# Kernel optimization log

Hardware: AMD Instinct MI355X
Metric: run time of the kernel (lower is better)

Reference implementation:

```python
import jax, jax.numpy as jnp
import numpy as np

B, T, V, D, H, HS, FF, L = 4, 1024, 32000, 1024, 16, 64, 4096, 8
STD = 0.02

def _ln(x, g, b, eps=1e-5):
    m = x.mean(-1, keepdims=True)
    v = ((x - m) ** 2).mean(-1, keepdims=True)
    return (x - m) / jnp.sqrt(v + eps) * g + b

def setup_inputs() -> dict:
    key = jax.random.key(0)
    ks = jax.random.split(key, 16)
    n = lambda k, shp: jax.random.normal(k, shp, dtype=jnp.float32) * STD
    inp = {
        "idx": jax.random.randint(ks[0], (B, T), 0, V),
        "tok_emb": n(ks[1], (V, D)),
        "pos_emb": n(ks[2], (T, D)),
        # per-layer stacked attention weights; [D, H, HS] per layer (no bias)
        "Wq": n(ks[3], (L, D, H, HS)),
        "Wk": n(ks[4], (L, D, H, HS)),
        "Wv": n(ks[5], (L, D, H, HS)),
        "Wp": n(ks[6], (L, H * HS, D)),
        "bp": jnp.zeros((L, D), jnp.float32),
        "ln1_g": jnp.ones((L, D), jnp.float32),
        "ln1_b": jnp.zeros((L, D), jnp.float32),
        "ln2_g": jnp.ones((L, D), jnp.float32),
        "ln2_b": jnp.zeros((L, D), jnp.float32),
        "W1": n(ks[7], (L, D, FF)),
        "b1": jnp.zeros((L, FF), jnp.float32),
        "W2": n(ks[8], (L, FF, D)),
        "b2": jnp.zeros((L, D), jnp.float32),
        "lnf_g": jnp.ones((D,), jnp.float32),
        "lnf_b": jnp.zeros((D,), jnp.float32),
        "Wlm": n(ks[9], (D, V)),
        "blm": jnp.zeros((V,), jnp.float32),
    }
    return inp

def reference(idx, tok_emb, pos_emb, Wq, Wk, Wv, Wp, bp, ln1_g, ln1_b,
              ln2_g, ln2_b, W1, b1, W2, b2, lnf_g, lnf_b, Wlm, blm):
    Bb, Tt = idx.shape
    x = tok_emb[idx] + pos_emb[:Tt]                      # [B,T,D]
    causal = jnp.tril(jnp.ones((Tt, Tt), bool))          # tril mask
    for l in range(L):
        xn = _ln(x, ln1_g[l], ln1_b[l])
        q = jnp.einsum('btd,dhk->bhtk', xn, Wq[l])
        k = jnp.einsum('btd,dhk->bhtk', xn, Wk[l])
        v = jnp.einsum('btd,dhk->bhtk', xn, Wv[l])
        w = jnp.einsum('bhtk,bhsk->bhts', q, k) * (HS ** -0.5)
        w = jnp.where(causal, w, -jnp.inf)
        w = jax.nn.softmax(w, axis=-1)
        o = jnp.einsum('bhts,bhsk->bhtk', w, v)
        o = o.transpose(0, 2, 1, 3).reshape(Bb, Tt, H * HS)  # concat heads
        x = x + o @ Wp[l] + bp[l]
        xn = _ln(x, ln2_g[l], ln2_b[l])
        x = x + jax.nn.relu(xn @ W1[l] + b1[l]) @ W2[l] + b2[l]
    x = _ln(x, lnf_g, lnf_b)
    logits = x @ Wlm + blm                               # [B,T,V]
    return logits
```

## Files before the change

kernel.cpp:

```cpp
#include <hip/hip_runtime.h>
#include <cstdint>

typedef __attribute__((ext_vector_type(4))) float f32x4;
typedef __attribute__((ext_vector_type(8))) short s16x8;
typedef __attribute__((ext_vector_type(4))) short s16x4;
typedef unsigned short u16;
typedef unsigned int u32;
typedef __attribute__((address_space(1))) void gas_void;
typedef __attribute__((address_space(3))) void las_void;

#define B_ 4
#define T_ 1024
#define V_ 32000
#define D_ 1024
#define H_ 16
#define HS_ 64
#define FF_ 4096
#define L_ 8
#define BT_ (B_ * T_)

__device__ __forceinline__ float bf2f(u16 h) { return __uint_as_float(((u32)h) << 16); }
__device__ __forceinline__ u16 f2bf(float f) {
  u32 u = __float_as_uint(f);
  u += 0x7fffu + ((u >> 16) & 1u);
  return (u16)(u >> 16);
}

__device__ __forceinline__ void gld16(const void* g, void* l) {
  __builtin_amdgcn_global_load_lds((gas_void*)(uintptr_t)g,
                                   (las_void*)(u32)(uintptr_t)l, 16, 0, 0);
}


template <int EPI>
__global__ __launch_bounds__(512, 2) void gemm256(
    const u16* __restrict__ A, const u16* __restrict__ Bt,
    const float* __restrict__ bias, float* Cf, u16* Cb,
    int M, int N, int K, int nrowb) {
  __shared__ u16 lds[2][2][2][8192];
  const int tid = threadIdx.x;
  const int lane = tid & 63;
  const int lr = lane & 15, hi = lane >> 4;
  const int wid = tid >> 6;
  const int wm128 = (wid >> 2) << 7;
  const int wn64 = (wid & 3) << 6;
  const int logical = ((int)blockIdx.x & 7) * ((int)gridDim.x >> 3) + ((int)blockIdx.x >> 3);
  const int row0 = (logical % nrowb) << 8;
  const int col0 = (logical / nrowb) << 8;
  const int NT = K >> 6;
  const int srow = tid >> 2;
  const int schunk = tid & 3;
  const int xo = ((hi + (lr >> 1)) & 3) << 4;

  f32x4 acc[32];
#pragma unroll
  for (int i = 0; i < 32; ++i) acc[i] = f32x4{0.f, 0.f, 0.f, 0.f};
  s16x8 bfr[4];

#define VMW(N) asm volatile("s_waitcnt vmcnt(" #N ")" ::: "memory")

#define STG(DB, DK, OP, KT)                                                    \
  {                                                                            \
    const u16* sp_ = (OP) ? Bt : A;                                            \
    const int base_ = (OP) ? col0 : row0;                                      \
    const int c0_ = ((KT) << 6) + ((DK) << 5);                                 \
    _Pragma("unroll")                                                          \
    for (int sh_ = 0; sh_ < 2; ++sh_) {                                        \
      const int rr_ = (sh_ << 7) + srow;                                       \
      const int ko_ = ((schunk - (rr_ >> 1)) & 3) << 3;                        \
      gld16(sp_ + (size_t)(base_ + rr_) * K + c0_ + ko_,                       \
            (char*)&lds[DB][DK][OP][0] + (sh_ << 13) + (wid << 10));           \
    }                                                                          \
  }

#define PHASE(BUF, MH, KS, LOADB, STG_STMT, VM_STMT)                           \
  {                                                                            \
    __builtin_amdgcn_sched_barrier(0);                                         \
    const char* As_ = (const char*)&lds[BUF][KS][0][0];                        \
    const char* Bs_ = (const char*)&lds[BUF][KS][1][0];                        \
    const int ra_ = wm128 + ((MH) << 6) + lr;                                  \
    s16x8 af_[4];                                                              \
    _Pragma("unroll")                                                          \
    for (int q_ = 0; q_ < 4; ++q_)                                             \
      af_[q_] = *(const s16x8*)(As_ + ((ra_ + (q_ << 4)) << 6) + xo);          \
    if (LOADB) {                                                               \
      _Pragma("unroll")                                                        \
      for (int q_ = 0; q_ < 4; ++q_)                                           \
        bfr[q_] = *(const s16x8*)(Bs_ + ((wn64 + lr + (q_ << 4)) << 6) + xo);  \
    }                                                                          \
    STG_STMT;                                                                  \
    __builtin_amdgcn_sched_barrier(0);                                         \
    __builtin_amdgcn_s_barrier();                                              \
    asm volatile("s_waitcnt lgkmcnt(0)" ::: "memory");                         \
    __builtin_amdgcn_sched_barrier(0);                                         \
    __builtin_amdgcn_s_setprio(1);                                             \
    _Pragma("unroll")                                                          \
    for (int mi_ = 0; mi_ < 4; ++mi_) {                                        \
      _Pragma("unroll")                                                        \
      for (int nj_ = 0; nj_ < 4; ++nj_)                                        \
        acc[((MH)*4 + mi_) * 4 + nj_] = __builtin_amdgcn_mfma_f32_16x16x32_bf16( \
            af_[mi_], bfr[nj_], acc[((MH)*4 + mi_) * 4 + nj_], 0, 0, 0);       \
    }                                                                          \
    __builtin_amdgcn_s_setprio(0);                                             \
    __builtin_amdgcn_sched_barrier(0);                                         \
    VM_STMT;                                                                   \
    __builtin_amdgcn_s_barrier();                                              \
  }

  STG(0, 0, 0, 0)
  STG(0, 0, 1, 0)
  STG(0, 1, 0, 0)
  STG(0, 1, 1, 0)
  STG(1, 0, 0, 1)
  STG(1, 0, 1, 1)
  VMW(8);
  __builtin_amdgcn_s_barrier();

  const int NI = NT >> 1;
  for (int it = 0; it < NI - 1; ++it) {
    const int t1 = 2 * it + 1, t2 = 2 * it + 2, t3 = 2 * it + 3;
    PHASE(0, 0, 0, 1, STG(1, 1, 0, t1), )
    PHASE(0, 1, 0, 0, STG(1, 1, 1, t1), VMW(6))
    PHASE(0, 0, 1, 1, STG(0, 0, 0, t2), )
    PHASE(0, 1, 1, 0, STG(0, 0, 1, t2), VMW(6))
    PHASE(1, 0, 0, 1, STG(0, 1, 0, t2), )
    PHASE(1, 1, 0, 0, STG(0, 1, 1, t2), VMW(6))
    PHASE(1, 0, 1, 1, STG(1, 0, 0, t3), )
    PHASE(1, 1, 1, 0, STG(1, 0, 1, t3), VMW(6))
  }
  {
    PHASE(0, 0, 0, 1, STG(1, 1, 0, NT - 1), )
    PHASE(0, 1, 0, 0, STG(1, 1, 1, NT - 1), VMW(8))
    PHASE(0, 0, 1, 1, (void)0, )
    PHASE(0, 1, 1, 0, (void)0, VMW(4))
    PHASE(1, 0, 0, 1, (void)0, )
    PHASE(1, 1, 0, 0, (void)0, VMW(0))
    PHASE(1, 0, 1, 1, (void)0, )
    PHASE(1, 1, 1, 0, (void)0, )
  }
#undef PHASE
#undef STG
#undef VMW

  const int gr0 = row0 + wm128;
  const int gc0 = col0 + wn64;
#pragma unroll
  for (int nj = 0; nj < 4; ++nj) {
    const int col = gc0 + (nj << 4) + lr;
    const float bv = (EPI != 0) ? bias[col] : 0.f;
#pragma unroll
    for (int mi = 0; mi < 8; ++mi) {
#pragma unroll
      for (int rg = 0; rg < 4; ++rg) {
        const int row = gr0 + (mi << 4) + (hi << 2) + rg;
        const size_t off = (size_t)row * N + col;
        float val = acc[mi * 4 + nj][rg] + bv;
        if constexpr (EPI == 2) val = fmaxf(val, 0.f);
        if constexpr (EPI == 0 || EPI == 2) Cb[off] = f2bf(val);
        else Cf[off] = val;
      }
    }
  }
}

template <int EPI>
__global__ __launch_bounds__(256) void gemm_bt(
    const u16* __restrict__ A, const u16* __restrict__ Bt,
    const float* __restrict__ bias, float* Cf, u16* Cb,
    int M, int N, int K) {
  __shared__ u16 lds[2][2][4096];
  const int tid = threadIdx.x;
  const int lane = tid & 63;
  const int lr = lane & 15, hi = lane >> 4;
  const int wid = tid >> 6;
  const int wm = wid >> 1, wn = wid & 1;
  const int row0 = blockIdx.y << 7, col0 = blockIdx.x << 7;
  const int NT = K >> 5;
  const int wbase = (tid & ~63) << 4;
  const int xo = ((hi + (lr >> 1)) & 3) << 4;

  f32x4 acc[4][4];
#pragma unroll
  for (int i = 0; i < 4; ++i)
#pragma unroll
    for (int j = 0; j < 4; ++j) acc[i][j] = f32x4{0.f, 0.f, 0.f, 0.f};

  auto stage = [&](int buf, int kt) {
#pragma unroll
    for (int c = 0; c < 2; ++c) {
      const int o = (c << 12) + (tid << 4);
      const int r = o >> 6;
      const int ko = ((((o >> 4) & 3) - (r >> 1)) & 3) << 3;
      gld16(A + (size_t)(row0 + r) * K + (kt << 5) + ko,
            (char*)&lds[buf][0][0] + (c << 12) + wbase);
      gld16(Bt + (size_t)(col0 + r) * K + (kt << 5) + ko,
            (char*)&lds[buf][1][0] + (c << 12) + wbase);
    }
  };

  stage(0, 0);
  __syncthreads();
  int cur = 0;
  for (int kt = 0; kt < NT; ++kt) {
    if (kt + 1 < NT) stage(cur ^ 1, kt + 1);
    const char* As = (const char*)&lds[cur][0][0];
    const char* Bs = (const char*)&lds[cur][1][0];
    s16x8 af[4], bfr[4];
#pragma unroll
    for (int i = 0; i < 4; ++i) {
      const int ra = (wm << 6) + (i << 4) + lr;
      af[i] = *(const s16x8*)(As + (ra << 6) + xo);
      const int rb = (wn << 6) + (i << 4) + lr;
      bfr[i] = *(const s16x8*)(Bs + (rb << 6) + xo);
    }
#pragma unroll
    for (int i = 0; i < 4; ++i)
#pragma unroll
      for (int j = 0; j < 4; ++j)
        acc[i][j] =
            __builtin_amdgcn_mfma_f32_16x16x32_bf16(af[i], bfr[j], acc[i][j], 0, 0, 0);
    __syncthreads();
    cur ^= 1;
  }

  const int gr = row0 + (wm << 6);
  const int gc = col0 + (wn << 6);
#pragma unroll
  for (int j = 0; j < 4; ++j) {
    const int col = gc + (j << 4) + lr;
    const float bv = (EPI != 0) ? bias[col] : 0.f;
#pragma unroll
    for (int i = 0; i < 4; ++i) {
#pragma unroll
      for (int rg = 0; rg < 4; ++rg) {
        const int row = gr + (i << 4) + (hi << 2) + rg;
        const size_t off = (size_t)row * N + col;
        float val = acc[i][j][rg] + bv;
        if constexpr (EPI == 1) val += Cf[off];
        if constexpr (EPI == 2) val = fmaxf(val, 0.f);
        if constexpr (EPI == 0 || EPI == 2) Cb[off] = f2bf(val);
        else Cf[off] = val;
      }
    }
  }
}

__global__ __launch_bounds__(256) void ln_kernel(const float* __restrict__ x,
                                                 const float* __restrict__ gw,
                                                 const float* __restrict__ bw,
                                                 u16* __restrict__ out) {
  const int lane = threadIdx.x & 63;
  const size_t r = ((size_t)blockIdx.x << 2) + (threadIdx.x >> 6);
  const float* xp = x + (r << 10);
  f32x4 v[4];
  float s = 0.f, q = 0.f;
#pragma unroll
  for (int j = 0; j < 4; ++j) {
    v[j] = *(const f32x4*)(xp + (lane << 2) + (j << 8));
#pragma unroll
    for (int e = 0; e < 4; ++e) {
      s += v[j][e];
      q += v[j][e] * v[j][e];
    }
  }
#pragma unroll
  for (int off = 32; off; off >>= 1) {
    s += __shfl_xor(s, off);
    q += __shfl_xor(q, off);
  }
  const float mean = s * (1.f / 1024.f);
  const float var = q * (1.f / 1024.f) - mean * mean;
  const float rstd = rsqrtf(var + 1e-5f);
  u16* op = out + (r << 10);
#pragma unroll
  for (int j = 0; j < 4; ++j) {
    const f32x4 g4 = *(const f32x4*)(gw + (lane << 2) + (j << 8));
    const f32x4 b4 = *(const f32x4*)(bw + (lane << 2) + (j << 8));
    s16x4 o4;
#pragma unroll
    for (int e = 0; e < 4; ++e)
      o4[e] = (short)f2bf((v[j][e] - mean) * rstd * g4[e] + b4[e]);
    *(s16x4*)(op + (lane << 2) + (j << 8)) = o4;
  }
}

__global__ __launch_bounds__(256) void embed_kernel(const int* __restrict__ idx,
                                                    const float* __restrict__ tok,
                                                    const float* __restrict__ pos,
                                                    float* __restrict__ x) {
  const int r = blockIdx.x, tid = threadIdx.x;
  const int t = r & (T_ - 1);
  const int tk = idx[r];
  f32x4 a = *(const f32x4*)(tok + ((size_t)tk << 10) + (tid << 2));
  f32x4 p = *(const f32x4*)(pos + ((size_t)t << 10) + (tid << 2));
  *(f32x4*)(x + ((size_t)r << 10) + (tid << 2)) = a + p;
}

#define TCONV_BODY(SRC, DST, KK, NN)                                           \
  {                                                                            \
    __shared__ float tile[32][33];                                             \
    const int tx = threadIdx.x & 31, ty = threadIdx.x >> 5;                    \
    const int n0 = blockIdx.x << 5, k0 = blockIdx.y << 5;                      \
    _Pragma("unroll")                                                          \
    for (int i = 0; i < 32; i += 8)                                            \
      tile[ty + i][tx] = (SRC)[(size_t)(k0 + ty + i) * (NN) + n0 + tx];        \
    __syncthreads();                                                           \
    _Pragma("unroll")                                                          \
    for (int i = 0; i < 32; i += 8)                                            \
      (DST)[(size_t)(n0 + ty + i) * (KK) + k0 + tx] = f2bf(tile[tx][ty + i]);  \
  }

__global__ __launch_bounds__(256) void tconv_qkvp(
    const float* __restrict__ Wq, const float* __restrict__ Wk,
    const float* __restrict__ Wv, const float* __restrict__ Wp,
    u16* __restrict__ WqkvT, u16* __restrict__ WpT) {
  const int z = blockIdx.z;
  const int l = z >> 2, m = z & 3;
  const float* src;
  u16* dst;
  if (m == 0) { src = Wq + (size_t)l * D_ * D_; dst = WqkvT + (size_t)l * 3072 * D_; }
  else if (m == 1) { src = Wk + (size_t)l * D_ * D_; dst = WqkvT + (size_t)l * 3072 * D_ + D_ * D_; }
  else if (m == 2) { src = Wv + (size_t)l * D_ * D_; dst = WqkvT + (size_t)l * 3072 * D_ + 2 * D_ * D_; }
  else { src = Wp + (size_t)l * D_ * D_; dst = WpT + (size_t)l * D_ * D_; }
  TCONV_BODY(src, dst, D_, D_)
}

__global__ __launch_bounds__(256) void tconv_w1(const float* __restrict__ W1,
                                                u16* __restrict__ W1T) {
  const int l = blockIdx.z;
  TCONV_BODY(W1 + (size_t)l * D_ * FF_, W1T + (size_t)l * FF_ * D_, D_, FF_)
}

__global__ __launch_bounds__(256) void tconv_w2(const float* __restrict__ W2,
                                                u16* __restrict__ W2T) {
  const int l = blockIdx.z;
  TCONV_BODY(W2 + (size_t)l * FF_ * D_, W2T + (size_t)l * D_ * FF_, FF_, D_)
}

__global__ __launch_bounds__(256) void tconv_kernel(const float* __restrict__ src,
                                                    u16* __restrict__ dst, int K, int N) {
  TCONV_BODY(src, dst, K, N)
}

__global__ __launch_bounds__(256) void fattn_kernel(const u16* __restrict__ qkv,
                                                    u16* __restrict__ o) {
  const int flat = (int)blockIdx.x + ((int)blockIdx.y << 4) + ((int)blockIdx.z << 8);
  const int xcd = flat & 7, seq = flat >> 3;
  const int pair = (xcd << 3) + (seq >> 4);
  const int qt = seq & 15;
  const int h = pair & 15, b = pair >> 4;
  const int tid = threadIdx.x;
  const int lane = tid & 63;
  const int lr = lane & 15, hi = lane >> 4;
  const int w = tid >> 6;
  __shared__ alignas(16) u16 Kl[2][4096];
  __shared__ alignas(16) u16 Vt[2][4096];

  const size_t bT = (size_t)(b * T_);
  const int q_row = (qt << 6) + (w << 4) + lr;
  const size_t qbase = (bT + q_row) * 3072 + (h << 6);
  s16x8 aq[2];
  aq[0] = *(const s16x8*)(qkv + qbase + hi * 8);
  aq[1] = *(const s16x8*)(qkv + qbase + 32 + hi * 8);

  f32x4 ofr[4];
#pragma unroll
  for (int j = 0; j < 4; ++j) ofr[j] = f32x4{0.f, 0.f, 0.f, 0.f};
  float mrun = -1e30f, lsum = 0.f;

  uint4 vr0, vr1;

#define STAGEK(BUF, KT)                                                        \
  {                                                                            \
    _Pragma("unroll")                                                          \
    for (int sh_ = 0; sh_ < 2; ++sh_) {                                        \
      const int ob_ = (sh_ << 12) + (tid << 4);                                \
      const int r_ = ob_ >> 7;                                                 \
      const int il_ = (ob_ & 127) ^ ((r_ & 7) << 4);                           \
      gld16(qkv + (bT + ((KT) << 6) + r_) * 3072 + 1024 + (h << 6) + (il_ >> 1), \
            (char*)&Kl[BUF][0] + (sh_ << 12) + ((tid & 192) << 4));            \
    }                                                                          \
  }
#define LOADV(KT)                                                              \
  {                                                                            \
    const u16* vs_ =                                                           \
        qkv + (bT + ((KT) << 6) + lane) * 3072 + 2048 + (h << 6) + (w << 4);   \
    vr0 = *(const uint4*)vs_;                                                  \
    vr1 = *(const uint4*)(vs_ + 8);                                            \
  }
#define WRITEV(BUF)                                                            \
  {                                                                            \
    const u16* p0_ = (const u16*)&vr0;                                         \
    const u16* p1_ = (const u16*)&vr1;                                         \
    _Pragma("unroll")                                                          \
    for (int j_ = 0; j_ < 8; ++j_) {                                           \
      const int sw_ = lane ^ (j_ << 3);                                        \
      Vt[BUF][(((w << 4) + j_) << 6) + sw_] = p0_[j_];                         \
      Vt[BUF][(((w << 4) + 8 + j_) << 6) + sw_] = p1_[j_];                     \
    }                                                                          \
  }

  STAGEK(0, 0)
  LOADV(0)
  asm volatile("s_waitcnt vmcnt(0)" ::: "memory");
  WRITEV(0)
  asm volatile("s_waitcnt lgkmcnt(0)" ::: "memory");
  __builtin_amdgcn_sched_barrier(0);
  __builtin_amdgcn_s_barrier();

  int cur = 0;
  for (int kt = 0; kt <= qt; ++kt) {
    if (kt < qt) {
      STAGEK(cur ^ 1, kt + 1)
      LOADV(kt + 1)
    }

    f32x4 s[4];
#pragma unroll
    for (int j = 0; j < 4; ++j) s[j] = f32x4{0.f, 0.f, 0.f, 0.f};
    __builtin_amdgcn_s_setprio(1);
#pragma unroll
    for (int kk = 0; kk < 2; ++kk)
#pragma unroll
      for (int j = 0; j < 4; ++j) {
        const int rb = (j << 4) + lr;
        const s16x8 bk = *(const s16x8*)((const char*)&Kl[cur][0] + (rb << 7) +
                                         ((((kk << 2) + hi) ^ (rb & 7)) << 4));
        s[j] = __builtin_amdgcn_mfma_f32_16x16x32_bf16(bk, aq[kk], s[j], 0, 0, 0);
      }
    __builtin_amdgcn_s_setprio(0);

    if (kt == qt) {
      const int qr = (w << 4) + lr;
#pragma unroll
      for (int j = 0; j < 4; ++j)
#pragma unroll
        for (int rg = 0; rg < 4; ++rg) {
          const int kvr = (j << 4) + (hi << 2) + rg;
          s[j][rg] = (kvr > qr) ? -1e30f : s[j][rg] * 0.125f;
        }
    } else {
#pragma unroll
      for (int j = 0; j < 4; ++j) s[j] = s[j] * 0.125f;
    }

    float mx = -1e30f;
#pragma unroll
    for (int j = 0; j < 4; ++j)
#pragma unroll
      for (int rg = 0; rg < 4; ++rg) mx = fmaxf(mx, s[j][rg]);
    mx = fmaxf(mx, __shfl_xor(mx, 16));
    mx = fmaxf(mx, __shfl_xor(mx, 32));
    const float mn = fmaxf(mrun, mx);
    const float sc = __expf(mrun - mn);
    mrun = mn;
    float rs = 0.f;
#pragma unroll
    for (int j = 0; j < 4; ++j)
#pragma unroll
      for (int rg = 0; rg < 4; ++rg) {
        const float e = __expf(s[j][rg] - mn);
        s[j][rg] = e;
        rs += e;
      }
    rs += __shfl_xor(rs, 16);
    rs += __shfl_xor(rs, 32);
    lsum = lsum * sc + rs;
    float scO[4];
#pragma unroll
    for (int rg = 0; rg < 4; ++rg) scO[rg] = __shfl(sc, (hi << 2) + rg);
#pragma unroll
    for (int j2 = 0; j2 < 4; ++j2)
#pragma unroll
      for (int rg = 0; rg < 4; ++rg) ofr[j2][rg] *= scO[rg];

    s16x8 pb[2];
#pragma unroll
    for (int kk = 0; kk < 2; ++kk)
#pragma unroll
      for (int i = 0; i < 4; ++i) {
        pb[kk][i] = (short)f2bf(s[2 * kk][i]);
        pb[kk][4 + i] = (short)f2bf(s[2 * kk + 1][i]);
      }

    __builtin_amdgcn_s_setprio(1);
#pragma unroll
    for (int kk = 0; kk < 2; ++kk)
#pragma unroll
      for (int j2 = 0; j2 < 4; ++j2) {
        const int drow = (j2 << 4) + lr;
        const int swz = (drow & 7) << 3;
        const int base = drow << 6;
        const s16x4 lo = *(const s16x4*)&Vt[cur][base + (((kk << 5) + (hi << 2)) ^ swz)];
        const s16x4 hv = *(const s16x4*)&Vt[cur][base + (((kk << 5) + 16 + (hi << 2)) ^ swz)];
        const s16x8 vb = __builtin_shufflevector(lo, hv, 0, 1, 2, 3, 4, 5, 6, 7);
        ofr[j2] = __builtin_amdgcn_mfma_f32_16x16x32_bf16(pb[kk], vb, ofr[j2], 0, 0, 0);
      }
    __builtin_amdgcn_s_setprio(0);

    if (kt < qt) {
      asm volatile("s_waitcnt vmcnt(0)" ::: "memory");
      WRITEV(cur ^ 1)
    }
    asm volatile("s_waitcnt lgkmcnt(0)" ::: "memory");
    __builtin_amdgcn_sched_barrier(0);
    __builtin_amdgcn_s_barrier();
    cur ^= 1;
  }

  const float rinv = 1.f / lsum;
  float rO[4];
#pragma unroll
  for (int rg = 0; rg < 4; ++rg) rO[rg] = __shfl(rinv, (hi << 2) + rg);
#pragma unroll
  for (int j2 = 0; j2 < 4; ++j2)
#pragma unroll
    for (int rg = 0; rg < 4; ++rg) {
      const int row = (qt << 6) + (w << 4) + (hi << 2) + rg;
      const int col = (h << 6) + (j2 << 4) + lr;
      o[(bT + row) * 1024 + col] = f2bf(ofr[j2][rg] * rO[rg]);
    }
#undef STAGEK
#undef LOADV
#undef WRITEV
}

extern "C" void kernel_launch(void* const* d_in, const int* in_sizes, int n_in,
                              void* d_out, int out_size, void* d_ws, size_t ws_size,
                              hipStream_t stream) {
  (void)in_sizes; (void)n_in; (void)out_size; (void)ws_size;
  const int* idx = (const int*)d_in[0];
  const float* tokE = (const float*)d_in[1];
  const float* posE = (const float*)d_in[2];
  const float* Wq = (const float*)d_in[3];
  const float* Wk = (const float*)d_in[4];
  const float* Wv = (const float*)d_in[5];
  const float* Wp = (const float*)d_in[6];
  const float* bp = (const float*)d_in[7];
  const float* ln1g = (const float*)d_in[8];
  const float* ln1b = (const float*)d_in[9];
  const float* ln2g = (const float*)d_in[10];
  const float* ln2b = (const float*)d_in[11];
  const float* W1 = (const float*)d_in[12];
  const float* b1 = (const float*)d_in[13];
  const float* W2 = (const float*)d_in[14];
  const float* b2 = (const float*)d_in[15];
  const float* lnfg = (const float*)d_in[16];
  const float* lnfb = (const float*)d_in[17];
  const float* Wlm = (const float*)d_in[18];
  const float* blm = (const float*)d_in[19];

  char* p = (char*)d_ws;
  float* x = (float*)p;   p += (size_t)BT_ * D_ * 4;
  u16* xn = (u16*)p;      p += (size_t)BT_ * D_ * 2;
  u16* qkv = (u16*)p;     p += (size_t)BT_ * 3072 * 2;
  u16* ob = (u16*)p;      p += (size_t)BT_ * D_ * 2;
  u16* hb = (u16*)p;      p += (size_t)BT_ * FF_ * 2;
  u16* WqkvT = (u16*)p;   p += (size_t)L_ * 3072 * D_ * 2;
  u16* WpT = (u16*)p;     p += (size_t)L_ * D_ * D_ * 2;
  u16* W1T = (u16*)p;     p += (size_t)L_ * FF_ * D_ * 2;
  u16* W2T = (u16*)p;     p += (size_t)L_ * D_ * FF_ * 2;
  u16* WlmT = (u16*)p;    p += (size_t)V_ * D_ * 2;

  dim3 blk(256);
  dim3 blk512(512);
  tconv_qkvp<<<dim3(32, 32, 32), blk, 0, stream>>>(Wq, Wk, Wv, Wp, WqkvT, WpT);
  tconv_w1<<<dim3(128, 32, 8), blk, 0, stream>>>(W1, W1T);
  tconv_w2<<<dim3(32, 128, 8), blk, 0, stream>>>(W2, W2T);
  tconv_kernel<<<dim3(1000, 32), blk, 0, stream>>>(Wlm, WlmT, D_, V_);

  embed_kernel<<<dim3(BT_), blk, 0, stream>>>(idx, tokE, posE, x);

  for (int l = 0; l < L_; ++l) {
    ln_kernel<<<dim3(BT_ / 4), blk, 0, stream>>>(x, ln1g + l * D_, ln1b + l * D_, xn);
    gemm_bt<0><<<dim3(24, 32), blk, 0, stream>>>(xn, WqkvT + (size_t)l * 3072 * D_,
                                                 nullptr, nullptr, qkv, BT_, 3072, D_);
    fattn_kernel<<<dim3(T_ / 64, H_, B_), blk, 0, stream>>>(qkv, ob);
    gemm_bt<1><<<dim3(8, 32), blk, 0, stream>>>(ob, WpT + (size_t)l * D_ * D_,
                                                bp + l * D_, x, nullptr, BT_, D_, D_);
    ln_kernel<<<dim3(BT_ / 4), blk, 0, stream>>>(x, ln2g + l * D_, ln2b + l * D_, xn);
    gemm256<2><<<dim3(256), blk512, 0, stream>>>(xn, W1T + (size_t)l * FF_ * D_,
                                                 b1 + l * FF_, nullptr, hb, BT_, FF_, D_, 16);
    gemm_bt<1><<<dim3(8, 32), blk, 0, stream>>>(hb, W2T + (size_t)l * D_ * FF_,
                                                b2 + l * D_, x, nullptr, BT_, D_, FF_);
  }
  ln_kernel<<<dim3(BT_ / 4), blk, 0, stream>>>(x, lnfg, lnfb, xn);
  gemm256<3><<<dim3(2000), blk512, 0, stream>>>(xn, WlmT, blm, (float*)d_out, nullptr,
                                                BT_, V_, D_, 16);
}
```

Baseline: 2.707 ms.

## Process 128-query tiles per 512-thread attention block sharing K/V staging

The flash-attention kernel now uses 8 waves covering 128 query rows per block instead of 4 waves and 64 rows, so each staged K/V tile in LDS is reused by twice as many queries. Staging work is split across 512 threads, and waves whose query rows lie entirely before a key tile skip its MFMA work. The softmax folds log2(e) into the scale and uses exp2f. This halves the grid to 512 blocks, which cuts redundant K/V loads but lowers parallelism and leaves idle waves at block barriers on the causal tail.

```diff
diff --git a/kernel.cpp b/kernel.cpp
--- a/kernel.cpp
+++ b/kernel.cpp
@@ -342,12 +342,12 @@
   TCONV_BODY(src, dst, K, N)
 }
 
-__global__ __launch_bounds__(256) void fattn_kernel(const u16* __restrict__ qkv,
+__global__ __launch_bounds__(512) void fattn_kernel(const u16* __restrict__ qkv,
                                                     u16* __restrict__ o) {
-  const int flat = (int)blockIdx.x + ((int)blockIdx.y << 4) + ((int)blockIdx.z << 8);
+  const int flat = (int)blockIdx.x;
   const int xcd = flat & 7, seq = flat >> 3;
-  const int pair = (xcd << 3) + (seq >> 4);
-  const int qt = seq & 15;
+  const int pair = (xcd << 3) + (seq >> 3);
+  const int qt = seq & 7;
   const int h = pair & 15, b = pair >> 4;
   const int tid = threadIdx.x;
   const int lane = tid & 63;
@@ -357,7 +357,8 @@
   __shared__ alignas(16) u16 Vt[2][4096];
 
   const size_t bT = (size_t)(b * T_);
-  const int q_row = (qt << 6) + (w << 4) + lr;
+  const int q_row = (qt << 7) + (w << 4) + lr;
+  const int qtw = (qt << 1) + (w >> 2);
   const size_t qbase = (bT + q_row) * 3072 + (h << 6);
   s16x8 aq[2];
   aq[0] = *(const s16x8*)(qkv + qbase + hi * 8);
@@ -367,37 +368,28 @@
 #pragma unroll
   for (int j = 0; j < 4; ++j) ofr[j] = f32x4{0.f, 0.f, 0.f, 0.f};
   float mrun = -1e30f, lsum = 0.f;
-
-  uint4 vr0, vr1;
+  const float SCL = 0.125f * 1.44269504f;
+
+  uint4 vr0;
 
 #define STAGEK(BUF, KT)                                                        \
   {                                                                            \
-    _Pragma("unroll")                                                          \
-    for (int sh_ = 0; sh_ < 2; ++sh_) {                                        \
-      const int ob_ = (sh_ << 12) + (tid << 4);                                \
-      const int r_ = ob_ >> 7;                                                 \
-      const int il_ = (ob_ & 127) ^ ((r_ & 7) << 4);                           \
-      gld16(qkv + (bT + ((KT) << 6) + r_) * 3072 + 1024 + (h << 6) + (il_ >> 1), \
-            (char*)&Kl[BUF][0] + (sh_ << 12) + ((tid & 192) << 4));            \
-    }                                                                          \
+    const int r_ = tid >> 3;                                                   \
+    const int il_ = (((tid & 7) << 4)) ^ ((r_ & 7) << 4);                      \
+    gld16(qkv + (bT + ((KT) << 6) + r_) * 3072 + 1024 + (h << 6) + (il_ >> 1), \
+          (char*)&Kl[BUF][0] + ((tid & 448) << 4));                            \
   }
 #define LOADV(KT)                                                              \
   {                                                                            \
-    const u16* vs_ =                                                           \
-        qkv + (bT + ((KT) << 6) + lane) * 3072 + 2048 + (h << 6) + (w << 4);   \
-    vr0 = *(const uint4*)vs_;                                                  \
-    vr1 = *(const uint4*)(vs_ + 8);                                            \
+    vr0 = *(const uint4*)(qkv + (bT + ((KT) << 6) + lane) * 3072 + 2048 +      \
+                          (h << 6) + (w << 3));                                \
   }
 #define WRITEV(BUF)                                                            \
   {                                                                            \
     const u16* p0_ = (const u16*)&vr0;                                         \
-    const u16* p1_ = (const u16*)&vr1;                                         \
     _Pragma("unroll")                                                          \
-    for (int j_ = 0; j_ < 8; ++j_) {                                           \
-      const int sw_ = lane ^ (j_ << 3);                                        \
-      Vt[BUF][(((w << 4) + j_) << 6) + sw_] = p0_[j_];                         \
-      Vt[BUF][(((w << 4) + 8 + j_) << 6) + sw_] = p1_[j_];                     \
-    }                                                                          \
+    for (int j_ = 0; j_ < 8; ++j_)                                             \
+      Vt[BUF][(((w << 3) + j_) << 6) + (lane ^ (j_ << 3))] = p0_[j_];          \
   }
 
   STAGEK(0, 0)
@@ -408,58 +400,64 @@
   __builtin_amdgcn_sched_barrier(0);
   __builtin_amdgcn_s_barrier();
 
+  const int nkt = (qt << 1) + 2;
   int cur = 0;
-  for (int kt = 0; kt <= qt; ++kt) {
-    if (kt < qt) {
+  for (int kt = 0; kt < nkt; ++kt) {
+    if (kt + 1 < nkt) {
       STAGEK(cur ^ 1, kt + 1)
       LOADV(kt + 1)
     }
 
+    const bool full = (kt > qtw);
     f32x4 s[4];
-#pragma unroll
-    for (int j = 0; j < 4; ++j) s[j] = f32x4{0.f, 0.f, 0.f, 0.f};
-    __builtin_amdgcn_s_setprio(1);
-#pragma unroll
-    for (int kk = 0; kk < 2; ++kk)
-#pragma unroll
-      for (int j = 0; j < 4; ++j) {
-        const int rb = (j << 4) + lr;
-        const s16x8 bk = *(const s16x8*)((const char*)&Kl[cur][0] + (rb << 7) +
-                                         ((((kk << 2) + hi) ^ (rb & 7)) << 4));
-        s[j] = __builtin_amdgcn_mfma_f32_16x16x32_bf16(bk, aq[kk], s[j], 0, 0, 0);
+    if (!full) {
+#pragma unroll
+      for (int j = 0; j < 4; ++j) s[j] = f32x4{0.f, 0.f, 0.f, 0.f};
+      __builtin_amdgcn_s_setprio(1);
+#pragma unroll
+      for (int kk = 0; kk < 2; ++kk)
+#pragma unroll
+        for (int j = 0; j < 4; ++j) {
+          const int rb = (j << 4) + lr;
+          const s16x8 bk = *(const s16x8*)((const char*)&Kl[cur][0] + (rb << 7) +
+                                           ((((kk << 2) + hi) ^ (rb & 7)) << 4));
+          s[j] = __builtin_amdgcn_mfma_f32_16x16x32_bf16(bk, aq[kk], s[j], 0, 0, 0);
+        }
+      __builtin_amdgcn_s_setprio(0);
+      if (kt == qtw) {
+        const int qr = q_row & 63;
+#pragma unroll
+        for (int j = 0; j < 4; ++j)
+#pragma unroll
+          for (int rg = 0; rg < 4; ++rg) {
+            const int kvr = (j << 4) + (hi << 2) + rg;
+            s[j][rg] = (kvr > qr) ? -1e30f : s[j][rg] * SCL;
+          }
+      } else {
+#pragma unroll
+        for (int j = 0; j < 4; ++j) s[j] = s[j] * SCL;
       }
-    __builtin_amdgcn_s_setprio(0);
-
-    if (kt == qt) {
-      const int qr = (w << 4) + lr;
-#pragma unroll
-      for (int j = 0; j < 4; ++j)
-#pragma unroll
-        for (int rg = 0; rg < 4; ++rg) {
-          const int kvr = (j << 4) + (hi << 2) + rg;
-          s[j][rg] = (kvr > qr) ? -1e30f : s[j][rg] * 0.125f;
-        }
     } else {
 #pragma unroll
-      for (int j = 0; j < 4; ++j) s[j] = s[j] * 0.125f;
-    }
-
-    float mx = -1e30f;
-#pragma unroll
-    for (int j = 0; j < 4; ++j)
+      for (int j = 0; j < 4; ++j) s[j] = f32x4{-1e30f, -1e30f, -1e30f, -1e30f};
+    }
+
+    float mx = fmaxf(fmaxf(s[0][0], s[0][1]), fmaxf(s[0][2], s[0][3]));
+#pragma unroll
+    for (int j = 1; j < 4; ++j)
 #pragma unroll
       for (int rg = 0; rg < 4; ++rg) mx = fmaxf(mx, s[j][rg]);
     mx = fmaxf(mx, __shfl_xor(mx, 16));
     mx = fmaxf(mx, __shfl_xor(mx, 32));
     const float mn = fmaxf(mrun, mx);
-    const float sc = __expf(mrun - mn);
+    const float sc = exp2f(mrun - mn);
     mrun = mn;
     float rs = 0.f;
 #pragma unroll
     for (int j = 0; j < 4; ++j)
 #pragma unroll
       for (int rg = 0; rg < 4; ++rg) {
-        const float e = __expf(s[j][rg] - mn);
+        const float e = exp2f(s[j][rg] - mn);
         s[j][rg] = e;
         rs += e;
       }
@@ -474,31 +472,33 @@
 #pragma unroll
       for (int rg = 0; rg < 4; ++rg) ofr[j2][rg] *= scO[rg];
 
-    s16x8 pb[2];
-#pragma unroll
-    for (int kk = 0; kk < 2; ++kk)
-#pragma unroll
-      for (int i = 0; i < 4; ++i) {
-        pb[kk][i] = (short)f2bf(s[2 * kk][i]);
-        pb[kk][4 + i] = (short)f2bf(s[2 * kk + 1][i]);
-      }
-
-    __builtin_amdgcn_s_setprio(1);
-#pragma unroll
-    for (int kk = 0; kk < 2; ++kk)
-#pragma unroll
-      for (int j2 = 0; j2 < 4; ++j2) {
-        const int drow = (j2 << 4) + lr;
-        const int swz = (drow & 7) << 3;
-        const int base = drow << 6;
-        const s16x4 lo = *(const s16x4*)&Vt[cur][base + (((kk << 5) + (hi << 2)) ^ swz)];
-        const s16x4 hv = *(const s16x4*)&Vt[cur][base + (((kk << 5) + 16 + (hi << 2)) ^ swz)];
-        const s16x8 vb = __builtin_shufflevector(lo, hv, 0, 1, 2, 3, 4, 5, 6, 7);
-        ofr[j2] = __builtin_amdgcn_mfma_f32_16x16x32_bf16(pb[kk], vb, ofr[j2], 0, 0, 0);
-      }
-    __builtin_amdgcn_s_setprio(0);
-
-    if (kt < qt) {
+    if (!full) {
+      s16x8 pb[2];
+#pragma unroll
+      for (int kk = 0; kk < 2; ++kk)
+#pragma unroll
+        for (int i = 0; i < 4; ++i) {
+          pb[kk][i] = (short)f2bf(s[2 * kk][i]);
+          pb[kk][4 + i] = (short)f2bf(s[2 * kk + 1][i]);
+        }
+
+      __builtin_amdgcn_s_setprio(1);
+#pragma unroll
+      for (int kk = 0; kk < 2; ++kk)
+#pragma unroll
+        for (int j2 = 0; j2 < 4; ++j2) {
+          const int drow = (j2 << 4) + lr;
+          const int swz = (drow & 7) << 3;
+          const int base = drow << 6;
+          const s16x4 lo = *(const s16x4*)&Vt[cur][base + (((kk << 5) + (hi << 2)) ^ swz)];
+          const s16x4 hv = *(const s16x4*)&Vt[cur][base + (((kk << 5) + 16 + (hi << 2)) ^ swz)];
+          const s16x8 vb = __builtin_shufflevector(lo, hv, 0, 1, 2, 3, 4, 5, 6, 7);
+          ofr[j2] = __builtin_amdgcn_mfma_f32_16x16x32_bf16(pb[kk], vb, ofr[j2], 0, 0, 0);
+        }
+      __builtin_amdgcn_s_setprio(0);
+    }
+
+    if (kt + 1 < nkt) {
       asm volatile("s_waitcnt vmcnt(0)" ::: "memory");
       WRITEV(cur ^ 1)
     }
@@ -516,7 +516,7 @@
   for (int j2 = 0; j2 < 4; ++j2)
 #pragma unroll
     for (int rg = 0; rg < 4; ++rg) {
-      const int row = (qt << 6) + (w << 4) + (hi << 2) + rg;
+      const int row = (qt << 7) + (w << 4) + (hi << 2) + rg;
       const int col = (h << 6) + (j2 << 4) + lr;
       o[(bT + row) * 1024 + col] = f2bf(ofr[j2][rg] * rO[rg]);
     }
@@ -575,7 +575,7 @@
     ln_kernel<<<dim3(BT_ / 4), blk, 0, stream>>>(x, ln1g + l * D_, ln1b + l * D_, xn);
     gemm_bt<0><<<dim3(24, 32), blk, 0, stream>>>(xn, WqkvT + (size_t)l * 3072 * D_,
                                                  nullptr, nullptr, qkv, BT_, 3072, D_);
-    fattn_kernel<<<dim3(T_ / 64, H_, B_), blk, 0, stream>>>(qkv, ob);
+    fattn_kernel<<<dim3(512), blk512, 0, stream>>>(qkv, ob);
     gemm_bt<1><<<dim3(8, 32), blk, 0, stream>>>(ob, WpT + (size_t)l * D_ * D_,
                                                 bp + l * D_, x, nullptr, BT_, D_, D_);
     ln_kernel<<<dim3(BT_ / 4), blk, 0, stream>>>(x, ln2g + l * D_, ln2b + l * D_, xn);
```

Result: no change. 2.720 ms (+0.5%).
